# Kernel tuning notes

Hardware: AMD Instinct MI355X
Metric: run time of the kernel (lower is better)

The kernel has to match this reference:

```python
import jax, jax.numpy as jnp
import numpy as np

N_ATOMS = 512
ATOM_SHAPE = (3, 3, 3)
SPARSE_ITERS = 128
FPB = 8  # features_per_band


def unit_norm(x, axis=-1, eps=1e-12):
    n = jnp.linalg.norm(x, axis=axis, keepdims=True)
    return x / jnp.maximum(n, eps)


def best_fit(signal, atoms):
    # signal: [B, bands, time, per] ; atoms: [n_atoms, 3,3,3]
    B, bands, time, per = signal.shape
    sig = signal[:, None]  # [B,1,bands,time,per]
    # pad (0,2) on last three dims
    sig = jnp.pad(sig, ((0, 0), (0, 0), (0, 2), (0, 2), (0, 2)))
    # conv3d correlation: lax conv with NCDHW / OIDHW
    fm = jax.lax.conv_general_dilated(
        sig, atoms[:, None], window_strides=(1, 1, 1), padding='VALID',
        dimension_numbers=('NCDHW', 'OIDHW', 'NCDHW'))  # [B, n_atoms, bands, time, per]
    flat = fm.reshape(B, -1)
    idx = jnp.argmax(flat, axis=-1)
    val = jnp.take_along_axis(flat, idx[:, None], axis=-1)[:, 0]
    # unflatten index -> (atom, b, c, d)
    fshape = fm.shape[1:]
    a_i = idx // (fshape[1] * fshape[2] * fshape[3])
    rem = idx % (fshape[1] * fshape[2] * fshape[3])
    b_i = rem // (fshape[2] * fshape[3])
    rem = rem % (fshape[2] * fshape[3])
    c_i = rem // fshape[3]
    d_i = rem % fshape[3]

    def per_batch(sig_b, a, b, c, dd, v):
        # sig_b: padded [bands+2, time+2, per+2]
        atom = atoms[a] * v  # [3,3,3]
        # Since conv output spatial extent = input extent (valid over padded),
        # max offsets b,c,d <= dims-1 of padded-2, slice always fits fully.
        patch = jax.lax.dynamic_slice(sig_b, (b, c, dd), ATOM_SHAPE)
        return jax.lax.dynamic_update_slice(sig_b, patch - atom, (b, c, dd))

    sig2 = jax.vmap(per_batch)(sig[:, 0], a_i, b_i, c_i, d_i, val)
    return sig2[:, :bands, :time, :per]


def sparse_code(signal, atoms):
    def body(res, _):
        return best_fit(res, atoms), None
    res, _ = jax.lax.scan(body, signal, None, length=SPARSE_ITERS)
    return res


def layer_norm(x, g, b, eps=1e-5):
    m = jnp.mean(x, axis=-1, keepdims=True)
    v = jnp.var(x, axis=-1, keepdims=True)
    return (x - m) / jnp.sqrt(v + eps) * g + b


def batch_norm(x, g, b, eps=1e-5):
    # x: [B, C, T]; training-mode batch stats over (B, T)
    m = jnp.mean(x, axis=(0, 2), keepdims=True)
    v = jnp.var(x, axis=(0, 2), keepdims=True)
    return (x - m) / jnp.sqrt(v + eps) * g[None, :, None] + b[None, :, None]


def conv1d(x, w, b, pad):
    # x: [B,C,T], w: [O,I,K]
    y = jax.lax.conv_general_dilated(x, w, (1,), [(pad, pad)],
                                     dimension_numbers=('NCT', 'OIT', 'NCT'))
    return y + b[None, :, None]


def upsample4(x):
    # nearest, scale 4 along time
    return jnp.repeat(x, 4, axis=-1)


def setup_inputs() -> dict:
    key = jax.random.key(0)
    ks = jax.random.split(key, 24)
    w = 0.05
    x = jax.random.normal(ks[0], (4, 128, 128, 257), dtype=jnp.float32)
    d = jax.random.uniform(ks[1], (N_ATOMS, 27), minval=-1, maxval=1)
    atoms = unit_norm(d, axis=-1).reshape(N_ATOMS, *ATOM_SHAPE)
    inp = {
        'x': x,
        'atoms': atoms,
        'embed_w': jax.random.normal(ks[2], (257, FPB)) * w,
        'embed_b': jnp.zeros((FPB,)),
        # LinearOutputStack(1024, 3, out 1024, LayerNorm): 3 hidden-ish linears
        'ctx_w1': jax.random.normal(ks[3], (1024, 1024)) * w,
        'ctx_b1': jnp.zeros((1024,)),
        'ctx_g1': jnp.ones((1024,)), 'ctx_be1': jnp.zeros((1024,)),
        'ctx_w2': jax.random.normal(ks[4], (1024, 1024)) * w,
        'ctx_b2': jnp.zeros((1024,)),
        'ctx_g2': jnp.ones((1024,)), 'ctx_be2': jnp.zeros((1024,)),
        'ctx_w3': jax.random.normal(ks[5], (1024, 1024)) * w,
        'ctx_b3': jnp.zeros((1024,)),
        # up stack conv weights
        'up_w1': jax.random.normal(ks[6], (512, 1024, 7)) * w,
        'up_b1': jnp.zeros((512,)), 'bn_g1': jnp.ones((512,)), 'bn_b1': jnp.zeros((512,)),
        'up_w2': jax.random.normal(ks[7], (256, 512, 7)) * w,
        'up_b2': jnp.zeros((256,)), 'bn_g2': jnp.ones((256,)), 'bn_b2': jnp.zeros((256,)),
        'up_w3': jax.random.normal(ks[8], (128, 256, 7)) * w,
        'up_b3': jnp.zeros((128,)), 'bn_g3': jnp.ones((128,)), 'bn_b3': jnp.zeros((128,)),
        'up_w4': jax.random.normal(ks[9], (64, 128, 7)) * w,
        'up_b4': jnp.zeros((64,)), 'bn_g4': jnp.ones((64,)), 'bn_b4': jnp.zeros((64,)),
        'up_w5': jax.random.normal(ks[10], (1, 64, 7)) * w,
        'up_b5': jnp.zeros((1,)),
    }
    return inp


def reference(x, atoms, embed_w, embed_b,
              ctx_w1, ctx_b1, ctx_g1, ctx_be1,
              ctx_w2, ctx_b2, ctx_g2, ctx_be2,
              ctx_w3, ctx_b3,
              up_w1, up_b1, bn_g1, bn_b1,
              up_w2, up_b2, bn_g2, bn_b2,
              up_w3, up_b3, bn_g3, bn_b3,
              up_w4, up_b4, bn_g4, bn_b4,
              up_w5, up_b5):
    B, bands, time, per = x.shape
    # embed_features
    e = x @ embed_w + embed_b  # [B, bands, time, 8]
    # sparse coding (no_grad in original; result discarded but computed)
    _res = jax.lax.stop_gradient(sparse_code(e, atoms))
    encoded = jnp.transpose(e, (0, 3, 1, 2)).reshape(B, FPB * bands, time)  # [B,1024,T]
    # context
    ctx = jnp.sum(encoded, axis=-1)  # [B,1024]
    h = layer_norm(jax.nn.leaky_relu(ctx @ ctx_w1 + ctx_b1, 0.2), ctx_g1, ctx_be1)
    h = layer_norm(jax.nn.leaky_relu(h @ ctx_w2 + ctx_b2, 0.2), ctx_g2, ctx_be2)
    ctx_out = h @ ctx_w3 + ctx_b3
    # generate (up stack)
    y = jax.nn.leaky_relu(batch_norm(conv1d(encoded, up_w1, up_b1, 3), bn_g1, bn_b1), 0.2)
    y = upsample4(y)
    y = jax.nn.leaky_relu(batch_norm(conv1d(y, up_w2, up_b2, 3), bn_g2, bn_b2), 0.2)
    y = upsample4(y)
    y = jax.nn.leaky_relu(batch_norm(conv1d(y, up_w3, up_b3, 3), bn_g3, bn_b3), 0.2)
    y = upsample4(y)
    y = jax.nn.leaky_relu(batch_norm(conv1d(y, up_w4, up_b4, 3), bn_g4, bn_b4), 0.2)
    y = upsample4(y)
    y = conv1d(y, up_w5, up_b5, 3)  # [B,1,T*256]
    # reverb approximated as identity mix (ReverbGenerator source unavailable)
    return y, ctx_out
```

## Files before the change

### kernel.cpp

```cpp
#include <hip/hip_runtime.h>
#include <hip/hip_bf16.h>

using sh8   = __attribute__((ext_vector_type(8))) short;
using sh4   = __attribute__((ext_vector_type(4))) short;
using f32x4 = __attribute__((ext_vector_type(4))) float;

#define DEV __device__ __forceinline__

DEV float leaky(float x) { return x >= 0.f ? x : 0.2f * x; }

DEV unsigned short f2bf(float f) {
  unsigned u = __float_as_uint(f);
  u += 0x7FFF + ((u >> 16) & 1);
  return (unsigned short)(u >> 16);
}
DEV float bf2f(unsigned short b) { return __uint_as_float(((unsigned)b) << 16); }

template<int Cout, int Cin>
DEV void pack7_body(const float* __restrict__ w, unsigned short* __restrict__ wp, int blk) {
  constexpr long plane = (long)(Cin >> 5) * Cout * 32;
  int tid = blk * 256 + threadIdx.x;
  if (tid >= Cout * Cin) return;
  int co = tid / Cin, ci = tid - co * Cin;
  const float* src = w + (long)tid * 7;
  unsigned short* dst = wp + ((long)(ci >> 5) * Cout + co) * 32 + (ci & 31);
  #pragma unroll
  for (int k = 0; k < 7; ++k) dst[k * plane] = f2bf(src[k]);
}
template<int Cout, int Cin>
DEV void packph_body(const float* __restrict__ w, unsigned short* __restrict__ wp, int blk) {
  constexpr long plane = (long)(Cin >> 5) * Cout * 32;
  int tid = blk * 256 + threadIdx.x;
  if (tid >= Cout * Cin) return;
  int co = tid / Cin, ci = tid - co * Cin;
  float wk[7];
  #pragma unroll
  for (int k = 0; k < 7; ++k) wk[k] = w[(long)tid * 7 + k];
  unsigned short* dst = wp + ((long)(ci >> 5) * Cout + co) * 32 + (ci & 31);
  #pragma unroll
  for (int p = 0; p < 4; ++p) {
    #pragma unroll
    for (int d = 0; d < 3; ++d) {
      float s = 0.f;
      #pragma unroll
      for (int k = 0; k < 7; ++k) if (((p + k + 1) >> 2) == d) s += wk[k];
      dst[(p * 3 + d) * plane] = f2bf(s);
    }
  }
}
__global__ __launch_bounds__(256)
void pack_all(const float* __restrict__ w1, const float* __restrict__ w2,
              const float* __restrict__ w3, const float* __restrict__ w4,
              unsigned short* __restrict__ wbuf) {
  int blk = blockIdx.x;
  if (blk < 2048)      pack7_body<512, 1024>(w1, wbuf, blk);
  else if (blk < 2560) packph_body<256, 512>(w2, wbuf + 3670016, blk - 2048);
  else if (blk < 2688) packph_body<128, 256>(w3, wbuf + 5242880, blk - 2560);
  else                 packph_body<64, 128>(w4, wbuf + 5636096, blk - 2688);
}

__global__ __launch_bounds__(256)
void embed_mfma(const float* __restrict__ x, const float* __restrict__ ew,
                const float* __restrict__ eb, unsigned short* __restrict__ encbf,
                float* __restrict__ ctx) {
  __shared__ unsigned short W16[257 * 16];
  __shared__ unsigned short sv[64 * 260];
  __shared__ float ctxred[4][8];
  const int tid = threadIdx.x;
  const int bid = blockIdx.x;
  const long rowbase = (long)bid * 128;
  const int b = bid >> 7, band = bid & 127;

  for (int i = tid; i < 257 * 16; i += 256) {
    int p = i >> 4, f = i & 15;
    W16[i] = (f < 8) ? f2bf(ew[p * 8 + f]) : (unsigned short)0;
  }
  {
    const float* src = x + rowbase * 257;
    #pragma unroll
    for (int u = 0; u < 8; ++u) {
      float tmp[8];
      #pragma unroll
      for (int v = 0; v < 8; ++v) tmp[v] = src[tid + (u * 8 + v) * 256];
      #pragma unroll
      for (int v = 0; v < 8; ++v) {
        int idx = tid + (u * 8 + v) * 256;
        int r = idx / 257, c = idx - r * 257;
        sv[r * 260 + c] = f2bf(tmp[v]);
      }
    }
    if (tid < 64) sv[63 * 260 + 193 + tid] = f2bf(src[16384 + tid]);
  }
  __syncthreads();

  const int w = tid >> 6, lane = tid & 63;
  const int m = lane & 15, g = lane >> 4;

  sh8 breg[8];
  #pragma unroll
  for (int kk = 0; kk < 8; ++kk) {
    #pragma unroll
    for (int j = 0; j < 8; ++j)
      breg[kk][j] = (short)W16[(kk * 32 + g * 8 + j) * 16 + m];
  }
  const float w256 = bf2f(W16[256 * 16 + m]);
  const float ebf = (m < 8) ? eb[m] : 0.f;

  float ctx_acc = 0.f;
  #pragma unroll
  for (int ph = 0; ph < 2; ++ph) {
    if (ph) {
      __syncthreads();
      const float* src = x + (rowbase + 64) * 257;
      #pragma unroll
      for (int u = 0; u < 8; ++u) {
        float tmp[8];
        #pragma unroll
        for (int v = 0; v < 8; ++v) tmp[v] = src[tid + (u * 8 + v) * 256];
        #pragma unroll
        for (int v = 0; v < 8; ++v) {
          int idx = tid + (u * 8 + v) * 256;
          int r = idx / 257, c = idx - r * 257;
          sv[r * 260 + c] = f2bf(tmp[v]);
        }
      }
      if (tid < 64) sv[63 * 260 + 193 + tid] = f2bf(src[16384 + tid]);
      __syncthreads();
    }
    f32x4 acc = {0.f, 0.f, 0.f, 0.f};
    const unsigned short* bp0 = sv + (w * 16 + m) * 260 + g * 8;
    #pragma unroll
    for (int kk = 0; kk < 8; ++kk) {
      sh4 lo = *(const sh4*)(bp0 + kk * 32);
      sh4 hi = *(const sh4*)(bp0 + kk * 32 + 4);
      sh8 afr;
      afr[0] = lo[0]; afr[1] = lo[1]; afr[2] = lo[2]; afr[3] = lo[3];
      afr[4] = hi[0]; afr[5] = hi[1]; afr[6] = hi[2]; afr[7] = hi[3];
      acc = __builtin_amdgcn_mfma_f32_16x16x32_bf16(afr, breg[kk], acc, 0, 0, 0);
    }
    const int t0 = ph * 64 + w * 16;
    unsigned short pk[4];
    #pragma unroll
    for (int r = 0; r < 4; ++r) {
      float xv = bf2f(sv[(w * 16 + g * 4 + r) * 260 + 256]);
      float e = acc[r] + xv * w256 + ebf;
      pk[r] = f2bf(e);
      ctx_acc += e;
    }
    if (m < 8) {
      long o = ((long)b * 1024 + m * 128 + band) * 128 + t0 + g * 4;
      *(ushort4*)(encbf + o) = make_ushort4(pk[0], pk[1], pk[2], pk[3]);
    }
  }
  ctx_acc += __shfl_xor(ctx_acc, 16);
  ctx_acc += __shfl_xor(ctx_acc, 32);
  if (lane < 8) ctxred[w][lane] = ctx_acc;
  __syncthreads();
  if (tid < 8) {
    float sv2 = ctxred[0][tid] + ctxred[1][tid] + ctxred[2][tid] + ctxred[3][tid];
    ctx[(long)b * 1024 + tid * 128 + band] = sv2;
  }
}

__global__ void gemm_p(const float* __restrict__ h, const float* __restrict__ w,
                       float* __restrict__ gpart) {
  __shared__ float hl[4][128];
  __shared__ float red[8][4][32];
  const int kc = blockIdx.y, jb = blockIdx.x, k0 = kc * 128;
  for (int i = threadIdx.x; i < 512; i += 256) {
    int bb = i >> 7, kk = i & 127;
    hl[bb][kk] = h[(bb << 10) + k0 + kk];
  }
  __syncthreads();
  const int jl = threadIdx.x & 31, kq = threadIdx.x >> 5;
  const int j = jb * 32 + jl;
  float a0 = 0, a1 = 0, a2 = 0, a3 = 0;
  const float* wp = w + (long)(k0 + kq * 16) * 1024 + j;
  #pragma unroll
  for (int k = 0; k < 16; ++k) {
    float wv = wp[(long)k * 1024];
    a0 += hl[0][kq * 16 + k] * wv;
    a1 += hl[1][kq * 16 + k] * wv;
    a2 += hl[2][kq * 16 + k] * wv;
    a3 += hl[3][kq * 16 + k] * wv;
  }
  red[kq][0][jl] = a0; red[kq][1][jl] = a1; red[kq][2][jl] = a2; red[kq][3][jl] = a3;
  __syncthreads();
  if (threadIdx.x < 128) {
    int bb = threadIdx.x >> 5, j2 = threadIdx.x & 31;
    float s = 0;
    #pragma unroll
    for (int q = 0; q < 8; ++q) s += red[q][bb][j2];
    gpart[((long)kc * 4 + bb) * 1024 + jb * 32 + j2] = s;
  }
}

__global__ void lnsum_kernel(const float* __restrict__ gpart, const float* __restrict__ bias,
                             const float* __restrict__ g, const float* __restrict__ be,
                             float* __restrict__ out) {
  int b = blockIdx.x;
  __shared__ float buf[1024];
  __shared__ float rs[4], rq[4];
  float s = 0, q = 0;
  #pragma unroll
  for (int i = 0; i < 4; ++i) {
    int j = threadIdx.x + i * 256;
    float v = bias[j];
    #pragma unroll
    for (int kc = 0; kc < 8; ++kc) v += gpart[((long)kc * 4 + b) * 1024 + j];
    v = leaky(v);
    buf[j] = v; s += v; q += v * v;
  }
  #pragma unroll
  for (int off = 32; off; off >>= 1) { s += __shfl_down(s, off); q += __shfl_down(q, off); }
  int wid = threadIdx.x >> 6, lane = threadIdx.x & 63;
  if (lane == 0) { rs[wid] = s; rq[wid] = q; }
  __syncthreads();
  float S = rs[0] + rs[1] + rs[2] + rs[3];
  float Q = rq[0] + rq[1] + rq[2] + rq[3];
  float mean = S * (1.f / 1024.f);
  float var = Q * (1.f / 1024.f) - mean * mean;
  float rstd = rsqrtf(var + 1e-5f);
  #pragma unroll
  for (int i = 0; i < 4; ++i) {
    int j = threadIdx.x + i * 256;
    out[b * 1024 + j] = (buf[j] - mean) * rstd * g[j] + be[j];
  }
}

__global__ void fin_kernel(const float* __restrict__ gpart, const float* __restrict__ bias,
                           float* __restrict__ out) {
  int i = blockIdx.x * 256 + threadIdx.x;
  int b = i >> 10, j = i & 1023;
  float v = bias[j];
  #pragma unroll
  for (int kc = 0; kc < 8; ++kc) v += gpart[((long)kc * 4 + b) * 1024 + j];
  out[i] = v;
}

template<int UPS, int SPLITK>
__global__ __launch_bounds__(256, 2)
void conv_mfma(const unsigned short* __restrict__ act,
               const unsigned short* __restrict__ wpack,
               float* __restrict__ outp,
               int Cin, int Cout, int Tout) {
  constexpr int NC = (UPS == 1) ? 70 : 18;
  const int Tin = Tout / UPS;
  const int cpb = Cin / SPLITK;
  const int ncib = cpb >> 5;
  const int nCibTot = Cin >> 5;
  const int nco = Cout >> 6, nt = Tout >> 6;

  int bid = blockIdx.x;
  const int sk = bid % SPLITK; bid /= SPLITK;
  const int tt = bid % nt;  bid /= nt;
  const int cot = bid % nco; bid /= nco;
  const int b = bid;
  const int t0 = tt << 6, co0 = cot << 6;
  const int ci0 = sk * cpb;

  extern __shared__ unsigned short lin[];

  const unsigned short* actb = act + ((long)b * Cin + ci0) * Tin;
  const int u_base = (UPS == 1) ? (t0 - 3) : ((t0 >> 2) - 1);
  const int total = cpb * NC;
  for (int i = threadIdx.x; i < total; i += 256) {
    int ci = i / NC, ul = i - ci * NC;
    int u = u_base + ul;
    unsigned short v = 0;
    if (u >= 0 && u < Tin) v = actb[(long)ci * Tin + u];
    lin[((ci >> 5) * NC + ul) * 40 + (ci & 31)] = v;
  }
  __syncthreads();

  const int lane = threadIdx.x & 63, w = threadIdx.x >> 6;
  const int m = lane & 15, g = lane >> 4;

  int boff[28];
  #pragma unroll
  for (int s = 0; s < 4; ++s) {
    #pragma unroll
    for (int k = 0; k < 7; ++k) {
      int row = (UPS == 1) ? (s * 16 + m + k)
                           : (s * 4 + ((m + k + 9) >> 2) - 2);
      boff[s * 7 + k] = row * 40 + g * 8;
    }
  }

  const long wlane = ((long)(co0 + w * 16 + m) * 4 + g) * 8;

  f32x4 acc[4];
  #pragma unroll
  for (int s = 0; s < 4; ++s) { acc[s][0] = 0.f; acc[s][1] = 0.f; acc[s][2] = 0.f; acc[s][3] = 0.f; }

  for (int cib = 0; cib < ncib; ++cib) {
    const unsigned short* lb = lin + cib * (NC * 40);
    const int cg = (ci0 >> 5) + cib;
    sh8 a[7];
    #pragma unroll
    for (int k = 0; k < 7; ++k)
      a[k] = *(const sh8*)(wpack + (long)(k * nCibTot + cg) * Cout * 32 + wlane);
    #pragma unroll
    for (int k = 0; k < 7; ++k) {
      #pragma unroll
      for (int s = 0; s < 4; ++s) {
        sh8 bfr = *(const sh8*)(lb + boff[s * 7 + k]);
        acc[s] = __builtin_amdgcn_mfma_f32_16x16x32_bf16(a[k], bfr, acc[s], 0, 0, 0);
      }
    }
  }

  float* op = outp + (((long)sk * 4 + b) * Cout + (co0 + w * 16 + g * 4)) * (long)Tout + t0 + m;
  #pragma unroll
  for (int r = 0; r < 4; ++r) {
    #pragma unroll
    for (int s = 0; s < 4; ++s)
      op[(long)r * Tout + s * 16] = acc[s][r];
  }
}

template<int SPLITK>
__global__ __launch_bounds__(256, 2)
void conv_ph(const float* __restrict__ csum_in, const float* __restrict__ sp,
             const float* __restrict__ g, const float* __restrict__ be,
             const unsigned short* __restrict__ wpack,
             float* __restrict__ outp,
             int Cin, int Cout, int Tin) {
  const int Tout = Tin << 2;
  const int cpb = Cin / SPLITK;
  const int ncib = cpb >> 5;
  const int nCibTot = Cin >> 5;
  const int nco = Cout >> 6, ntu = Tin >> 6;

  int bid = blockIdx.x;
  const int sk = bid % SPLITK; bid /= SPLITK;
  const int tu = bid % ntu; bid /= ntu;
  const int cot = bid % nco; bid /= nco;
  const int b = bid;
  const int u0 = tu << 6, co0 = cot << 6;
  const int ci0 = sk * cpb;

  extern __shared__ unsigned short lin[];
  __shared__ float ssc[64], ssh[64];

  if (threadIdx.x < cpb) {
    int c = ci0 + threadIdx.x;
    float S = sp[c * 4] + sp[c * 4 + 1] + sp[c * 4 + 2] + sp[c * 4 + 3];
    float Q = sp[Cin * 4 + c * 4] + sp[Cin * 4 + c * 4 + 1] + sp[Cin * 4 + c * 4 + 2] + sp[Cin * 4 + c * 4 + 3];
    float n = 4.f * (float)Tin;
    float mean = S / n;
    float var = Q / n - mean * mean;
    float sc = g[c] * rsqrtf(var + 1e-5f);
    ssc[threadIdx.x] = sc;
    ssh[threadIdx.x] = be[c] - mean * sc;
  }
  __syncthreads();

  const float* csb = csum_in + ((long)b * Cin + ci0) * Tin;
  const int total = cpb * 66;
  for (int i = threadIdx.x; i < total; i += 256) {
    int ci = i / 66, r = i - ci * 66;
    int u = u0 - 1 + r;
    unsigned short v = 0;
    if (u >= 0 && u < Tin) {
      float t = csb[(long)ci * Tin + u];
      v = f2bf(leaky(t * ssc[ci] + ssh[ci]));
    }
    lin[((ci >> 5) * 66 + r) * 40 + (ci & 31)] = v;
  }
  __syncthreads();

  const int lane = threadIdx.x & 63, w = threadIdx.x >> 6;
  const int m = lane & 15, g2 = lane >> 4;

  int boff[4][3];
  #pragma unroll
  for (int s = 0; s < 4; ++s)
    #pragma unroll
    for (int d = 0; d < 3; ++d)
      boff[s][d] = (s * 16 + m + d) * 40 + g2 * 8;

  const long wlane = ((long)(co0 + w * 16 + m)) * 32 + g2 * 8;

  f32x4 acc[4][4];
  #pragma unroll
  for (int s = 0; s < 4; ++s)
    #pragma unroll
    for (int p = 0; p < 4; ++p) { acc[s][p][0] = 0.f; acc[s][p][1] = 0.f; acc[s][p][2] = 0.f; acc[s][p][3] = 0.f; }

  for (int cib = 0; cib < ncib; ++cib) {
    const unsigned short* lb = lin + cib * (66 * 40);
    const int cg = (ci0 >> 5) + cib;
    sh8 a[12];
    #pragma unroll
    for (int pd = 0; pd < 12; ++pd)
      a[pd] = *(const sh8*)(wpack + ((long)(pd * nCibTot + cg) * Cout) * 32 + wlane);
    #pragma unroll
    for (int s = 0; s < 4; ++s) {
      sh8 b0 = *(const sh8*)(lb + boff[s][0]);
      sh8 b1 = *(const sh8*)(lb + boff[s][1]);
      sh8 b2 = *(const sh8*)(lb + boff[s][2]);
      acc[s][0] = __builtin_amdgcn_mfma_f32_16x16x32_bf16(a[0],  b0, acc[s][0], 0, 0, 0);
      acc[s][0] = __builtin_amdgcn_mfma_f32_16x16x32_bf16(a[1],  b1, acc[s][0], 0, 0, 0);
      acc[s][1] = __builtin_amdgcn_mfma_f32_16x16x32_bf16(a[3],  b0, acc[s][1], 0, 0, 0);
      acc[s][1] = __builtin_amdgcn_mfma_f32_16x16x32_bf16(a[4],  b1, acc[s][1], 0, 0, 0);
      acc[s][1] = __builtin_amdgcn_mfma_f32_16x16x32_bf16(a[5],  b2, acc[s][1], 0, 0, 0);
      acc[s][2] = __builtin_amdgcn_mfma_f32_16x16x32_bf16(a[6],  b0, acc[s][2], 0, 0, 0);
      acc[s][2] = __builtin_amdgcn_mfma_f32_16x16x32_bf16(a[7],  b1, acc[s][2], 0, 0, 0);
      acc[s][2] = __builtin_amdgcn_mfma_f32_16x16x32_bf16(a[8],  b2, acc[s][2], 0, 0, 0);
      acc[s][3] = __builtin_amdgcn_mfma_f32_16x16x32_bf16(a[10], b1, acc[s][3], 0, 0, 0);
      acc[s][3] = __builtin_amdgcn_mfma_f32_16x16x32_bf16(a[11], b2, acc[s][3], 0, 0, 0);
    }
  }

  float* op = outp + (((long)sk * 4 + b) * Cout + (co0 + w * 16 + g2 * 4)) * (long)Tout;
  #pragma unroll
  for (int r = 0; r < 4; ++r) {
    #pragma unroll
    for (int s = 0; s < 4; ++s) {
      float4 v4 = make_float4(acc[s][0][r], acc[s][1][r], acc[s][2][r], acc[s][3][r]);
      *(float4*)(op + (long)r * Tout + ((u0 + s * 16 + m) << 2)) = v4;
    }
  }
}

__global__ void bnsum_kernel(const float* __restrict__ p, float* __restrict__ sp,
                             float* __restrict__ csum, int C, int T, int SK) {
  int c = blockIdx.x, b = blockIdx.y;
  long stride = (long)4 * C * T;
  const float* r = p + ((long)b * C + c) * T;
  float* cw = csum + ((long)b * C + c) * T;
  float s = 0, q = 0;
  for (int t = threadIdx.x; t < T; t += 256) {
    float v = r[t];
    for (int k = 1; k < SK; ++k) v += r[t + k * stride];
    cw[t] = v;
    s += v; q += v * v;
  }
  #pragma unroll
  for (int off = 32; off; off >>= 1) { s += __shfl_down(s, off); q += __shfl_down(q, off); }
  __shared__ float rs[4], rq[4];
  int wid = threadIdx.x >> 6, lane = threadIdx.x & 63;
  if (lane == 0) { rs[wid] = s; rq[wid] = q; }
  __syncthreads();
  if (threadIdx.x == 0) {
    sp[c * 4 + b] = rs[0] + rs[1] + rs[2] + rs[3];
    sp[C * 4 + c * 4 + b] = rq[0] + rq[1] + rq[2] + rq[3];
  }
}

__global__ __launch_bounds__(256)
void conv5_kernel(const float* __restrict__ csum_in, const float* __restrict__ sp,
                  const float* __restrict__ g, const float* __restrict__ be,
                  const float* __restrict__ wgt, const float* __restrict__ bias,
                  float* __restrict__ out, int Tout) {
  __shared__ unsigned short sv[64 * 66];
  __shared__ float wph[64 * 13];
  __shared__ float ssc[64], ssh[64];

  const int b = blockIdx.y;
  const int u0 = blockIdx.x * 64;
  const int Tin = Tout >> 2;
  const int tid = threadIdx.x;

  {
    int ci = tid >> 2, pp = tid & 3;
    float s0 = 0, s1 = 0, s2 = 0;
    #pragma unroll
    for (int k = 0; k < 7; ++k) {
      int d = (pp - 3 + k + 4) >> 2;
      float wv = wgt[ci * 7 + k];
      if (d == 0) s0 += wv; else if (d == 1) s1 += wv; else s2 += wv;
    }
    wph[ci * 13 + pp * 3 + 0] = s0;
    wph[ci * 13 + pp * 3 + 1] = s1;
    wph[ci * 13 + pp * 3 + 2] = s2;
  }
  if (tid < 64) {
    float S = sp[tid * 4] + sp[tid * 4 + 1] + sp[tid * 4 + 2] + sp[tid * 4 + 3];
    float Q = sp[256 + tid * 4] + sp[256 + tid * 4 + 1] + sp[256 + tid * 4 + 2] + sp[256 + tid * 4 + 3];
    float n = 4.f * (float)Tin;
    float mean = S / n;
    float var = Q / n - mean * mean;
    float sc = g[tid] * rsqrtf(var + 1e-5f);
    ssc[tid] = sc;
    ssh[tid] = be[tid] - mean * sc;
  }
  __syncthreads();

  const float* inb = csum_in + (long)b * 64 * Tin;
  for (int i = tid; i < 64 * 66; i += 256) {
    int ci = i / 66, uu = i - ci * 66;
    int u = u0 - 1 + uu;
    unsigned short v = 0;
    if (u >= 0 && u < Tin) {
      float t = inb[(long)ci * Tin + u];
      v = f2bf(leaky(t * ssc[ci] + ssh[ci]));
    }
    sv[ci * 66 + uu] = v;
  }
  __syncthreads();

  const int ul = tid >> 2;
  const int chunk = tid & 3;
  float a0 = 0, a1 = 0, a2 = 0, a3 = 0;
  #pragma unroll
  for (int cc = 0; cc < 16; ++cc) {
    int ci = chunk * 16 + cc;
    float v0 = bf2f(sv[ci * 66 + ul]);
    float v1 = bf2f(sv[ci * 66 + ul + 1]);
    float v2 = bf2f(sv[ci * 66 + ul + 2]);
    const float* wp = wph + ci * 13;
    a0 += v0 * wp[0] + v1 * wp[1];
    a1 += v0 * wp[3] + v1 * wp[4] + v2 * wp[5];
    a2 += v0 * wp[6] + v1 * wp[7] + v2 * wp[8];
    a3 += v1 * wp[10] + v2 * wp[11];
  }
  #pragma unroll
  for (int msk = 1; msk <= 2; msk <<= 1) {
    a0 += __shfl_xor(a0, msk);
    a1 += __shfl_xor(a1, msk);
    a2 += __shfl_xor(a2, msk);
    a3 += __shfl_xor(a3, msk);
  }
  if (chunk == 0) {
    float bv = bias[0];
    float4 r = make_float4(a0 + bv, a1 + bv, a2 + bv, a3 + bv);
    *(float4*)(out + (long)b * Tout + (long)(u0 + ul) * 4) = r;
  }
}

extern "C" void kernel_launch(void* const* d_in, const int* in_sizes, int n_in,
                              void* d_out, int out_size, void* d_ws, size_t ws_size,
                              hipStream_t stream) {
  const float* x     = (const float*)d_in[0];
  const float* ew    = (const float*)d_in[2];
  const float* eb    = (const float*)d_in[3];
  const float* w1    = (const float*)d_in[4];
  const float* b1    = (const float*)d_in[5];
  const float* g1    = (const float*)d_in[6];
  const float* be1   = (const float*)d_in[7];
  const float* w2    = (const float*)d_in[8];
  const float* b2    = (const float*)d_in[9];
  const float* g2    = (const float*)d_in[10];
  const float* be2   = (const float*)d_in[11];
  const float* w3    = (const float*)d_in[12];
  const float* b3    = (const float*)d_in[13];
  const float* up_w1 = (const float*)d_in[14];
  const float* up_b1 = (const float*)d_in[15];
  const float* bn_g1 = (const float*)d_in[16];
  const float* bn_b1 = (const float*)d_in[17];
  const float* up_w2 = (const float*)d_in[18];
  const float* up_b2 = (const float*)d_in[19];
  const float* bn_g2 = (const float*)d_in[20];
  const float* bn_b2 = (const float*)d_in[21];
  const float* up_w3 = (const float*)d_in[22];
  const float* up_b3 = (const float*)d_in[23];
  const float* bn_g3 = (const float*)d_in[24];
  const float* bn_b3 = (const float*)d_in[25];
  const float* up_w4 = (const float*)d_in[26];
  const float* up_b4 = (const float*)d_in[27];
  const float* bn_g4 = (const float*)d_in[28];
  const float* bn_b4 = (const float*)d_in[29];
  const float* up_w5 = (const float*)d_in[30];
  const float* up_b5 = (const float*)d_in[31];

  float* out = (float*)d_out;

  float* ws = (float*)d_ws;
  float* ctxb   = ws;
  float* gpart  = ctxb + 4096;
  float* t2     = gpart + 32768;
  float* statsp = t2 + 4096;
  float* csum   = statsp + 4096;
  float* pbuf   = csum + 2097152;
  unsigned short* encbf = (unsigned short*)(pbuf + 4194304);
  unsigned short* wbuf  = encbf + 524288;

  pack_all<<<2720, 256, 0, stream>>>(up_w1, up_w2, up_w3, up_w4, wbuf);
  embed_mfma<<<512, 256, 0, stream>>>(x, ew, eb, encbf, ctxb);

  gemm_p<<<dim3(32, 8), 256, 0, stream>>>(ctxb, w1, gpart);
  lnsum_kernel<<<4, 256, 0, stream>>>(gpart, b1, g1, be1, t2);
  gemm_p<<<dim3(32, 8), 256, 0, stream>>>(t2, w2, gpart);
  lnsum_kernel<<<4, 256, 0, stream>>>(gpart, b2, g2, be2, t2);
  gemm_p<<<dim3(32, 8), 256, 0, stream>>>(t2, w3, gpart);
  fin_kernel<<<16, 256, 0, stream>>>(gpart, b3, out + 131072);

  conv_mfma<1, 8><<<512, 256, 22400, stream>>>(encbf, wbuf, pbuf, 1024, 512, 128);
  bnsum_kernel<<<dim3(512, 4), 256, 0, stream>>>(pbuf, statsp, csum, 512, 128, 8);

  conv_ph<8><<<256, 256, 10560, stream>>>(csum, statsp, bn_g1, bn_b1, wbuf + 3670016, pbuf, 512, 256, 128);
  bnsum_kernel<<<dim3(256, 4), 256, 0, stream>>>(pbuf, statsp, csum, 256, 512, 8);

  conv_ph<4><<<256, 256, 10560, stream>>>(csum, statsp, bn_g2, bn_b2, wbuf + 5242880, pbuf, 256, 128, 512);
  bnsum_kernel<<<dim3(128, 4), 256, 0, stream>>>(pbuf, statsp, csum, 128, 2048, 4);

  conv_ph<2><<<256, 256, 10560, stream>>>(csum, statsp, bn_g3, bn_b3, wbuf + 5636096, pbuf, 128, 64, 2048);
  bnsum_kernel<<<dim3(64, 4), 256, 0, stream>>>(pbuf, statsp, csum, 64, 8192, 2);

  conv5_kernel<<<dim3(128, 4), 256, 0, stream>>>(csum, statsp, bn_g4, bn_b4, up_w5, up_b5, out, 32768);
}
```

Measured before the change: 167.1 us.

## Load embed inputs directly into registers and split blocks per half

The embed kernel no longer stages x through shared memory. Each lane now loads its 8x8 fp32 values straight from global memory into registers and converts them to bf16 for the MFMA A-fragment. The grid doubles to 1024 blocks, each covering 64 rows, so there are more blocks in flight. The per-block context sums are written as two partials per band, and the first gemm_p adds them while loading. The direct loads are strided and uncoalesced (row stride 257 floats), which may cost more than the removed LDS round trip and barriers.

New measurement: 168.5 us. About the same (+0.9%).

```diff
diff --git a/kernel.cpp b/kernel.cpp
--- a/kernel.cpp
+++ b/kernel.cpp
@@ -2,7 +2,6 @@
 #include <hip/hip_bf16.h>
 
 using sh8   = __attribute__((ext_vector_type(8))) short;
-using sh4   = __attribute__((ext_vector_type(4))) short;
 using f32x4 = __attribute__((ext_vector_type(4))) float;
 
 #define DEV __device__ __forceinline__
@@ -62,35 +61,15 @@
 __global__ __launch_bounds__(256)
 void embed_mfma(const float* __restrict__ x, const float* __restrict__ ew,
                 const float* __restrict__ eb, unsigned short* __restrict__ encbf,
-                float* __restrict__ ctx) {
+                float* __restrict__ part) {
   __shared__ unsigned short W16[257 * 16];
-  __shared__ unsigned short sv[64 * 260];
   __shared__ float ctxred[4][8];
   const int tid = threadIdx.x;
-  const int bid = blockIdx.x;
-  const long rowbase = (long)bid * 128;
-  const int b = bid >> 7, band = bid & 127;
 
   for (int i = tid; i < 257 * 16; i += 256) {
     int p = i >> 4, f = i & 15;
     W16[i] = (f < 8) ? f2bf(ew[p * 8 + f]) : (unsigned short)0;
   }
-  {
-    const float* src = x + rowbase * 257;
-    #pragma unroll
-    for (int u = 0; u < 8; ++u) {
-      float tmp[8];
-      #pragma unroll
-      for (int v = 0; v < 8; ++v) tmp[v] = src[tid + (u * 8 + v) * 256];
-      #pragma unroll
-      for (int v = 0; v < 8; ++v) {
-        int idx = tid + (u * 8 + v) * 256;
-        int r = idx / 257, c = idx - r * 257;
-        sv[r * 260 + c] = f2bf(tmp[v]);
-      }
-    }
-    if (tid < 64) sv[63 * 260 + 193 + tid] = f2bf(src[16384 + tid]);
-  }
   __syncthreads();
 
   const int w = tid >> 6, lane = tid & 63;
@@ -106,62 +85,53 @@
   const float w256 = bf2f(W16[256 * 16 + m]);
   const float ebf = (m < 8) ? eb[m] : 0.f;
 
+  const int bid = blockIdx.x;
+  const long row0 = (long)bid * 64;
+  const int b = bid >> 8, band = (bid >> 1) & 127, half = bid & 1;
+  const int t0 = half * 64 + w * 16;
+
+  const float* xp = x + (row0 + w * 16 + m) * 257 + g * 8;
+  float vals[8][8];
+  #pragma unroll
+  for (int kk = 0; kk < 8; ++kk) {
+    #pragma unroll
+    for (int j = 0; j < 8; ++j)
+      vals[kk][j] = xp[kk * 32 + j];
+  }
+  f32x4 acc = {0.f, 0.f, 0.f, 0.f};
+  #pragma unroll
+  for (int kk = 0; kk < 8; ++kk) {
+    sh8 afr;
+    #pragma unroll
+    for (int j = 0; j < 8; ++j) afr[j] = (short)f2bf(vals[kk][j]);
+    acc = __builtin_amdgcn_mfma_f32_16x16x32_bf16(afr, breg[kk], acc, 0, 0, 0);
+  }
+
+  const float* xq = x + (row0 + w * 16 + g * 4) * 257 + 256;
   float ctx_acc = 0.f;
-  #pragma unroll
-  for (int ph = 0; ph < 2; ++ph) {
-    if (ph) {
-      __syncthreads();
-      const float* src = x + (rowbase + 64) * 257;
-      #pragma unroll
-      for (int u = 0; u < 8; ++u) {
-        float tmp[8];
-        #pragma unroll
-        for (int v = 0; v < 8; ++v) tmp[v] = src[tid + (u * 8 + v) * 256];
-        #pragma unroll
-        for (int v = 0; v < 8; ++v) {
-          int idx = tid + (u * 8 + v) * 256;
-          int r = idx / 257, c = idx - r * 257;
-          sv[r * 260 + c] = f2bf(tmp[v]);
-        }
-      }
-      if (tid < 64) sv[63 * 260 + 193 + tid] = f2bf(src[16384 + tid]);
-      __syncthreads();
-    }
-    f32x4 acc = {0.f, 0.f, 0.f, 0.f};
-    const unsigned short* bp0 = sv + (w * 16 + m) * 260 + g * 8;
-    #pragma unroll
-    for (int kk = 0; kk < 8; ++kk) {
-      sh4 lo = *(const sh4*)(bp0 + kk * 32);
-      sh4 hi = *(const sh4*)(bp0 + kk * 32 + 4);
-      sh8 afr;
-      afr[0] = lo[0]; afr[1] = lo[1]; afr[2] = lo[2]; afr[3] = lo[3];
-      afr[4] = hi[0]; afr[5] = hi[1]; afr[6] = hi[2]; afr[7] = hi[3];
-      acc = __builtin_amdgcn_mfma_f32_16x16x32_bf16(afr, breg[kk], acc, 0, 0, 0);
-    }
-    const int t0 = ph * 64 + w * 16;
-    unsigned short pk[4];
-    #pragma unroll
-    for (int r = 0; r < 4; ++r) {
-      float xv = bf2f(sv[(w * 16 + g * 4 + r) * 260 + 256]);
-      float e = acc[r] + xv * w256 + ebf;
-      pk[r] = f2bf(e);
-      ctx_acc += e;
-    }
-    if (m < 8) {
-      long o = ((long)b * 1024 + m * 128 + band) * 128 + t0 + g * 4;
-      *(ushort4*)(encbf + o) = make_ushort4(pk[0], pk[1], pk[2], pk[3]);
-    }
-  }
+  unsigned short pk[4];
+  #pragma unroll
+  for (int r = 0; r < 4; ++r) {
+    float e = acc[r] + xq[(long)r * 257] * w256 + ebf;
+    pk[r] = f2bf(e);
+    ctx_acc += e;
+  }
+  if (m < 8) {
+    long o = ((long)b * 1024 + m * 128 + band) * 128 + t0 + g * 4;
+    *(ushort4*)(encbf + o) = make_ushort4(pk[0], pk[1], pk[2], pk[3]);
+  }
+
   ctx_acc += __shfl_xor(ctx_acc, 16);
   ctx_acc += __shfl_xor(ctx_acc, 32);
   if (lane < 8) ctxred[w][lane] = ctx_acc;
   __syncthreads();
   if (tid < 8) {
-    float sv2 = ctxred[0][tid] + ctxred[1][tid] + ctxred[2][tid] + ctxred[3][tid];
-    ctx[(long)b * 1024 + tid * 128 + band] = sv2;
-  }
-}
-
+    float sv = ctxred[0][tid] + ctxred[1][tid] + ctxred[2][tid] + ctxred[3][tid];
+    part[((b * 1024 + tid * 128 + band) << 1) + half] = sv;
+  }
+}
+
+template<int SUM2>
 __global__ void gemm_p(const float* __restrict__ h, const float* __restrict__ w,
                        float* __restrict__ gpart) {
   __shared__ float hl[4][128];
@@ -169,7 +139,14 @@
   const int kc = blockIdx.y, jb = blockIdx.x, k0 = kc * 128;
   for (int i = threadIdx.x; i < 512; i += 256) {
     int bb = i >> 7, kk = i & 127;
-    hl[bb][kk] = h[(bb << 10) + k0 + kk];
+    float v;
+    if (SUM2) {
+      int base = ((bb << 10) + k0 + kk) << 1;
+      v = h[base] + h[base + 1];
+    } else {
+      v = h[(bb << 10) + k0 + kk];
+    }
+    hl[bb][kk] = v;
   }
   __syncthreads();
   const int jl = threadIdx.x & 31, kq = threadIdx.x >> 5;
@@ -568,8 +545,8 @@
   float* out = (float*)d_out;
 
   float* ws = (float*)d_ws;
-  float* ctxb   = ws;
-  float* gpart  = ctxb + 4096;
+  float* part   = ws;
+  float* gpart  = part + 8192;
   float* t2     = gpart + 32768;
   float* statsp = t2 + 4096;
   float* csum   = statsp + 4096;
@@ -578,13 +555,13 @@
   unsigned short* wbuf  = encbf + 524288;
 
   pack_all<<<2720, 256, 0, stream>>>(up_w1, up_w2, up_w3, up_w4, wbuf);
-  embed_mfma<<<512, 256, 0, stream>>>(x, ew, eb, encbf, ctxb);
-
-  gemm_p<<<dim3(32, 8), 256, 0, stream>>>(ctxb, w1, gpart);
+  embed_mfma<<<1024, 256, 0, stream>>>(x, ew, eb, encbf, part);
+
+  gemm_p<1><<<dim3(32, 8), 256, 0, stream>>>(part, w1, gpart);
   lnsum_kernel<<<4, 256, 0, stream>>>(gpart, b1, g1, be1, t2);
-  gemm_p<<<dim3(32, 8), 256, 0, stream>>>(t2, w2, gpart);
+  gemm_p<0><<<dim3(32, 8), 256, 0, stream>>>(t2, w2, gpart);
   lnsum_kernel<<<4, 256, 0, stream>>>(gpart, b2, g2, be2, t2);
-  gemm_p<<<dim3(32, 8), 256, 0, stream>>>(t2, w3, gpart);
+  gemm_p<0><<<dim3(32, 8), 256, 0, stream>>>(t2, w3, gpart);
   fin_kernel<<<16, 256, 0, stream>>>(gpart, b3, out + 131072);
 
   conv_mfma<1, 8><<<512, 256, 22400, stream>>>(encbf, wbuf, pbuf, 1024, 512, 128);
```
